# Kernel optimization log

Hardware: AMD Instinct MI355X
Metric: run time of the kernel (lower is better)

The kernel has to match this reference:

```python
import jax, jax.numpy as jnp
import numpy as np

N_CODES = 1024
D_CODE = 256
N_TOKENS = 131072
BETA = 0.25
DECAY = 0.97
EPS = 1e-05


def l2norm(x, axis=-1):
    # matches torch F.normalize(dim): x / max(||x||, 1e-12)
    n = jnp.sqrt(jnp.sum(x * x, axis=axis, keepdims=True))
    return x / jnp.maximum(n, 1e-12)


def setup_inputs() -> dict:
    key = jax.random.key(0)
    k1, k2, k3 = jax.random.split(key, 3)
    return {
        'z_e': jax.random.normal(k1, (N_TOKENS, D_CODE), dtype=jnp.float32),
        'codebook': jax.random.normal(k2, (N_CODES, D_CODE), dtype=jnp.float32),
        'ema_cluster_size': jnp.zeros((N_CODES,), dtype=jnp.float32),
        'ema_w': jax.random.normal(k3, (N_CODES, D_CODE), dtype=jnp.float32),
    }


def reference(z_e, codebook, ema_cluster_size, ema_w):
    z = l2norm(z_e, axis=1)                      # [N, d]
    cb = l2norm(codebook, axis=1)                # [K, d]
    # d = 2 - 2 * z @ cb.T ; argmin(d) == argmax(sim)
    sim = jnp.einsum('nd,kd->nk', z, cb)         # [N, K]
    codes = jnp.argmax(sim, axis=1)              # [N] int

    # EMA updates (no_grad in torch)
    counts = jnp.zeros((N_CODES,), z.dtype).at[codes].add(1.0)
    dw = jax.ops.segment_sum(z, codes, num_segments=N_CODES)  # onehot.T @ z
    new_cs = DECAY * ema_cluster_size + (1.0 - DECAY) * counts
    new_w = DECAY * ema_w + (1.0 - DECAY) * dw
    n = jnp.sum(new_cs)
    cluster_size = (new_cs + EPS) / (n + N_CODES * EPS) * n
    embed = l2norm(new_w / cluster_size[:, None], axis=1)
    # codebook.data.copy_(embed): value = embed, grad flows to codebook param
    new_cb = codebook + jax.lax.stop_gradient(embed - codebook)

    z_q = l2norm(new_cb[codes], axis=1)          # [N, d]
    vq_loss = BETA * jnp.mean((jax.lax.stop_gradient(z_e) - z_q) ** 2)
    z_q_out = z_e + jax.lax.stop_gradient(z_q - z_e)
    return (z_q_out, codes, vq_loss)
```

## Files before the change

kernel.cpp:

```cpp
#include <hip/hip_runtime.h>
#include <math.h>

#define N_TOK 131072
#define D 256
#define K_CODES 1024

typedef short bf16x8 __attribute__((ext_vector_type(8)));
typedef float f32x4 __attribute__((ext_vector_type(4)));

__device__ __forceinline__ unsigned short f2bf(float f) {
  unsigned x = __float_as_uint(f);
  unsigned r = x + 0x7fffu + ((x >> 16) & 1u);
  return (unsigned short)(r >> 16);
}

__global__ __launch_bounds__(256) void norm_cb_kernel(
    const float* __restrict__ cb, double* __restrict__ inv_nc64,
    unsigned short* __restrict__ cbbf) {
  const int c = blockIdx.x;
  const int d = threadIdx.x;
  const float v = cb[(size_t)c * D + d];
  double ssd = (double)v * (double)v;
#pragma unroll
  for (int o = 32; o; o >>= 1) ssd += __shfl_down(ssd, o, 64);
  __shared__ double red[4];
  if ((d & 63) == 0) red[d >> 6] = ssd;
  __syncthreads();
  const double tot = red[0] + red[1] + red[2] + red[3];
  const double inv = 1.0 / fmax(sqrt(tot), 1e-12);
  if (d == 0) inv_nc64[c] = inv;
  const int ctile = c >> 4, tk = c & 15;
  const int s = d >> 5, kg = (d >> 3) & 3, e = d & 7;
  cbbf[(((size_t)(ctile * 8 + s) * 64) + (kg * 16 + tk)) * 8 + e] =
      f2bf((float)((double)v * inv));
}

__global__ __launch_bounds__(512, 2) void vq_mfma_kernel(
    const float* __restrict__ z, const char* __restrict__ cbbf,
    float* __restrict__ out_codes, unsigned long long* __restrict__ cand2) {
  __shared__ __align__(16) char S[16384];
  __shared__ float norms[32];
  __shared__ int cand[32 * 8 * 3];
  __shared__ int clist[32 * 12];
  __shared__ float thrs[32];
  __shared__ int ccnt[32];

  const int tid = threadIdx.x;
  const int wv = tid >> 6;
  const int lane = tid & 63;
  const int t0b = blockIdx.x * 32;

  {
    const int tok = tid >> 4, sub = tid & 15;
    const float* zrow = z + (size_t)(t0b + tok) * D;
    float ss = 0.f;
#pragma unroll
    for (int i = 0; i < 2; ++i) {
      const int ku = sub + 16 * i;
      const float4 a = *(const float4*)(zrow + ku * 8);
      const float4 b = *(const float4*)(zrow + ku * 8 + 4);
      ss += a.x * a.x + a.y * a.y + a.z * a.z + a.w * a.w;
      ss += b.x * b.x + b.y * b.y + b.z * b.z + b.w * b.w;
      union { unsigned short h[8]; int4 v; } u;
      u.h[0] = f2bf(a.x); u.h[1] = f2bf(a.y); u.h[2] = f2bf(a.z); u.h[3] = f2bf(a.w);
      u.h[4] = f2bf(b.x); u.h[5] = f2bf(b.y); u.h[6] = f2bf(b.z); u.h[7] = f2bf(b.w);
      const int phys = (tok << 5) + (ku ^ (tok & 15));
      *(int4*)(S + ((size_t)phys << 4)) = u.v;
    }
    ss += __shfl_xor(ss, 1, 64);
    ss += __shfl_xor(ss, 2, 64);
    ss += __shfl_xor(ss, 4, 64);
    ss += __shfl_xor(ss, 8, 64);
    if (sub == 0) norms[tok] = sqrtf(ss);
  }
  __syncthreads();

  const int tk = lane & 15;
  const int kg = lane >> 4;

  f32x4 acc[2][8];
#pragma unroll
  for (int t = 0; t < 2; ++t)
#pragma unroll
    for (int c = 0; c < 8; ++c) acc[t][c] = (f32x4){0.f, 0.f, 0.f, 0.f};

  const char* cfb = cbbf + (size_t)wv * 65536 + (size_t)lane * 16;

#pragma unroll
  for (int s = 0; s < 8; ++s) {
    bf16x8 zf[2];
#pragma unroll
    for (int tt = 0; tt < 2; ++tt) {
      const int tok = tt * 16 + tk;
      const int ku = (s << 2) + kg;
      zf[tt] = *(const bf16x8*)(S + (((tok << 5) + (ku ^ (tok & 15))) << 4));
    }
    bf16x8 cf[8];
#pragma unroll
    for (int ct = 0; ct < 8; ++ct)
      cf[ct] = *(const bf16x8*)(cfb + ct * 8192 + s * 1024);
#pragma unroll
    for (int ct = 0; ct < 8; ++ct) {
      acc[0][ct] = __builtin_amdgcn_mfma_f32_16x16x32_bf16(cf[ct], zf[0], acc[0][ct], 0, 0, 0);
      acc[1][ct] = __builtin_amdgcn_mfma_f32_16x16x32_bf16(cf[ct], zf[1], acc[1][ct], 0, 0, 0);
    }
  }

#pragma unroll
  for (int tt = 0; tt < 2; ++tt) {
    float t1 = -3.0e38f, t2 = -3.0e38f;
    int i1 = 0;
#pragma unroll
    for (int ct = 0; ct < 8; ++ct)
#pragma unroll
      for (int r = 0; r < 4; ++r) {
        const float v = acc[tt][ct][r];
        const int k = (wv << 7) + (ct << 4) + (kg << 2) + r;
        if (v > t1) { t2 = t1; t1 = v; i1 = k; }
        else if (v > t2) t2 = v;
      }
#pragma unroll
    for (int off = 16; off <= 32; off <<= 1) {
      const float o1 = __shfl_xor(t1, off, 64);
      const int oi1 = __shfl_xor(i1, off, 64);
      const float o2 = __shfl_xor(t2, off, 64);
      const bool take = (o1 > t1) || (o1 == t1 && oi1 < i1);
      const float lo = take ? t1 : o1;
      t1 = take ? o1 : t1;
      i1 = take ? oi1 : i1;
      t2 = fmaxf(fmaxf(t2, o2), lo);
    }
    if (lane < 16) {
      int* p = cand + ((tt * 16 + lane) * 8 + wv) * 3;
      p[0] = __float_as_int(t1);
      p[1] = i1;
      p[2] = __float_as_int(t2);
    }
  }
  __syncthreads();

  if (tid < 32) {
    const float nrm = norms[tid];
    const float margin = 0.016f * nrm + 1.5e-3f;
    const int* base = cand + tid * 24;
    float v1 = -3.0e38f, v2 = -3.0e38f;
    int j1 = 0x7fffffff;
#pragma unroll
    for (int w = 0; w < 8; ++w) {
      const float a1 = __int_as_float(base[w * 3]);
      const int ai = base[w * 3 + 1];
      const float a2 = __int_as_float(base[w * 3 + 2]);
      const bool take = (a1 > v1) || (a1 == v1 && ai < j1);
      const float lo = take ? v1 : a1;
      v1 = take ? a1 : v1;
      j1 = take ? ai : j1;
      v2 = fmaxf(fmaxf(v2, a2), lo);
    }
    const float thr = v1 - margin;
    thrs[tid] = (v2 < thr) ? 3.0e38f : thr;
    ccnt[tid] = 0;
    out_codes[t0b + tid] = (float)j1;
  }
  __syncthreads();

#pragma unroll
  for (int tt = 0; tt < 2; ++tt) {
    const int tok = tt * 16 + tk;
    const float thr_t = thrs[tok];
#pragma unroll
    for (int ct = 0; ct < 8; ++ct)
#pragma unroll
      for (int r = 0; r < 4; ++r) {
        if (acc[tt][ct][r] >= thr_t) {
          const int pos = atomicAdd(&ccnt[tok], 1);
          if (pos < 12)
            clist[tok * 12 + pos] = (wv << 7) + (ct << 4) + (kg << 2) + r;
        }
      }
  }
  __syncthreads();

  if (tid < 32) {
    const int cnt = ccnt[tid];
    unsigned long long w0 = 0, w1 = 0;
    if (cnt > 0) {
      const int cc = cnt > 15 ? 15 : cnt;
      w0 = (unsigned long long)cc << 60;
      const int nst = cnt > 12 ? 12 : cnt;
      for (int j = 0; j < nst && j < 6; ++j)
        w0 |= ((unsigned long long)(clist[tid * 12 + j] & 1023)) << (10 * j);
      for (int j = 6; j < nst; ++j)
        w1 |= ((unsigned long long)(clist[tid * 12 + j] & 1023)) << (10 * (j - 6));
    }
    cand2[2 * (t0b + tid)] = w0;
    cand2[2 * (t0b + tid) + 1] = w1;
  }
}

__global__ __launch_bounds__(256) void recheck_kernel(
    const float* __restrict__ z, const float* __restrict__ cb,
    const double* __restrict__ inv_nc64,
    const unsigned long long* __restrict__ cand2,
    float* __restrict__ out_codes, int* __restrict__ ovf_list,
    int* __restrict__ ovf_cnt) {
  const int lane = threadIdx.x & 63;
  const int wid = (blockIdx.x * blockDim.x + threadIdx.x) >> 6;
  const int nw = (gridDim.x * blockDim.x) >> 6;
  for (int t = wid; t < N_TOK; t += nw) {
    const unsigned long long w0 = cand2[2 * t];
    if (w0 == 0ull) continue;
    const int cnt = (int)(w0 >> 60);
    if (cnt > 12) {
      if (lane == 0) ovf_list[atomicAdd(ovf_cnt, 1)] = t;
      continue;
    }
    const float4 zr = *(const float4*)(z + (size_t)t * D + lane * 4);
    const double z0 = zr.x, z1 = zr.y, z2 = zr.z, z3 = zr.w;
    const unsigned long long w1 = cand2[2 * t + 1];
    double best = -1.0e300;
    int bi = 0x7fffffff;
    for (int j = 0; j < cnt; ++j) {
      const int c = (j < 6) ? (int)((w0 >> (10 * j)) & 1023)
                            : (int)((w1 >> (10 * (j - 6))) & 1023);
      const float4 cr = *(const float4*)(cb + (size_t)c * D + lane * 4);
      double p = z0 * (double)cr.x + z1 * (double)cr.y +
                 z2 * (double)cr.z + z3 * (double)cr.w;
#pragma unroll
      for (int o = 32; o; o >>= 1) p += __shfl_xor(p, o, 64);
      p *= inv_nc64[c];
      if (p > best || (p == best && c < bi)) { best = p; bi = c; }
    }
    if (lane == 0) out_codes[t] = (float)bi;
  }
}

__global__ __launch_bounds__(256) void fullscan_kernel(
    const float* __restrict__ z, const float* __restrict__ cb,
    const double* __restrict__ inv_nc64, const int* __restrict__ ovf_list,
    const int* __restrict__ ovf_cnt, float* __restrict__ out_codes) {
  __shared__ float zs[256];
  __shared__ double bv[256];
  __shared__ int bis[256];
  const int n = *ovf_cnt;
  for (int i = blockIdx.x; i < n; i += gridDim.x) {
    const int t = ovf_list[i];
    zs[threadIdx.x] = z[(size_t)t * D + threadIdx.x];
    __syncthreads();
    double best = -1.0e300;
    int bidx = 0x7fffffff;
#pragma unroll
    for (int cc = 0; cc < 4; ++cc) {
      const int c = threadIdx.x + (cc << 8);
      const float4* crow = (const float4*)(cb + (size_t)c * D);
      double p = 0.0;
#pragma unroll 8
      for (int k4 = 0; k4 < 64; ++k4) {
        const float4 cv = crow[k4];
        p += (double)zs[4 * k4] * (double)cv.x +
             (double)zs[4 * k4 + 1] * (double)cv.y +
             (double)zs[4 * k4 + 2] * (double)cv.z +
             (double)zs[4 * k4 + 3] * (double)cv.w;
      }
      p *= inv_nc64[c];
      if (p > best || (p == best && c < bidx)) { best = p; bidx = c; }
    }
    bv[threadIdx.x] = best;
    bis[threadIdx.x] = bidx;
    __syncthreads();
    for (int s = 128; s; s >>= 1) {
      if (threadIdx.x < s) {
        const double ov = bv[threadIdx.x + s];
        const int oi = bis[threadIdx.x + s];
        if (ov > bv[threadIdx.x] ||
            (ov == bv[threadIdx.x] && oi < bis[threadIdx.x])) {
          bv[threadIdx.x] = ov;
          bis[threadIdx.x] = oi;
        }
      }
      __syncthreads();
    }
    if (threadIdx.x == 0) out_codes[t] = (float)bis[0];
    __syncthreads();
  }
}

__global__ __launch_bounds__(256) void inv_zn_kernel(
    const float* __restrict__ z, float* __restrict__ inv_zn) {
  const int lane = threadIdx.x & 63;
  const int wid = (blockIdx.x * blockDim.x + threadIdx.x) >> 6;
  const int nw = (gridDim.x * blockDim.x) >> 6;
  for (int t = wid; t < N_TOK; t += nw) {
    const float4 zr = *(const float4*)(z + (size_t)t * D + lane * 4);
    float ss = zr.x * zr.x + zr.y * zr.y + zr.z * zr.z + zr.w * zr.w;
#pragma unroll
    for (int o = 32; o; o >>= 1) ss += __shfl_xor(ss, o, 64);
    if (lane == 0) inv_zn[t] = 1.0f / fmaxf(sqrtf(ss), 1e-12f);
  }
}

__global__ __launch_bounds__(256) void hist_kernel(
    const float* __restrict__ codesf, int* __restrict__ hist) {
  const int t = blockIdx.x * 256 + threadIdx.x;
  if (t < N_TOK) atomicAdd(&hist[(int)codesf[t]], 1);
}

__global__ __launch_bounds__(256) void scan_kernel(
    const int* __restrict__ hist, int* __restrict__ offsets,
    int* __restrict__ cursor) {
  __shared__ int part[256];
  const int tid = threadIdx.x;
  int v[4];
  int s = 0;
#pragma unroll
  for (int j = 0; j < 4; ++j) {
    v[j] = hist[tid * 4 + j];
    s += v[j];
  }
  part[tid] = s;
  __syncthreads();
  for (int off = 1; off < 256; off <<= 1) {
    int x = (tid >= off) ? part[tid - off] : 0;
    __syncthreads();
    part[tid] += x;
    __syncthreads();
  }
  int excl = part[tid] - s;
#pragma unroll
  for (int j = 0; j < 4; ++j) {
    offsets[tid * 4 + j] = excl;
    cursor[tid * 4 + j] = excl;
    excl += v[j];
  }
  if (tid == 255) offsets[1024] = excl;
}

__global__ __launch_bounds__(256) void scatter_kernel(
    const float* __restrict__ codesf, int* __restrict__ cursor,
    int* __restrict__ tlist) {
  const int t = blockIdx.x * 256 + threadIdx.x;
  if (t < N_TOK) {
    const int c = (int)codesf[t];
    const int pos = atomicAdd(&cursor[c], 1);
    tlist[pos] = t;
  }
}

__global__ __launch_bounds__(256) void dw_build_kernel(
    const float* __restrict__ z, const int* __restrict__ tlist,
    const int* __restrict__ offsets, const float* __restrict__ inv_zn,
    const float* __restrict__ ema_w, float* __restrict__ embed) {
  const int c = blockIdx.x;
  const int d = threadIdx.x;
  const int i0 = offsets[c], i1 = offsets[c + 1];
  float sum = 0.f;
  for (int i = i0; i < i1; ++i) {
    const int t = tlist[i];
    sum += z[(size_t)t * D + d] * inv_zn[t];
  }
  const size_t idx = (size_t)c * D + d;
  const float w = 0.97f * ema_w[idx] + 0.03f * sum;
  float ss = w * w;
#pragma unroll
  for (int o = 32; o; o >>= 1) ss += __shfl_down(ss, o, 64);
  __shared__ float red[4];
  if ((d & 63) == 0) red[d >> 6] = ss;
  __syncthreads();
  const float tot = red[0] + red[1] + red[2] + red[3];
  embed[idx] = w / fmaxf(sqrtf(tot), 1e-12f);
}

__global__ __launch_bounds__(256) void gather_loss_kernel(
    const float* __restrict__ z, const float* __restrict__ embed,
    const float* __restrict__ codesf, float* __restrict__ out0,
    double* __restrict__ loss) {
  const size_t u0 = (size_t)blockIdx.x * 4096 + threadIdx.x;
  float part = 0.f;
#pragma unroll 4
  for (int i = 0; i < 16; ++i) {
    const size_t u = u0 + (size_t)i * 256;
    const size_t t = u >> 6;
    const int k4 = (int)(u & 63);
    const int code = (int)codesf[t];
    const float4 e = *(const float4*)(embed + (size_t)code * D + 4 * k4);
    const float4 ze = *(const float4*)(z + t * D + 4 * k4);
    *(float4*)(out0 + t * D + 4 * k4) = e;
    const float dx = ze.x - e.x, dy = ze.y - e.y;
    const float dz = ze.z - e.z, dw4 = ze.w - e.w;
    part += dx * dx + dy * dy + dz * dz + dw4 * dw4;
  }
#pragma unroll
  for (int o = 32; o; o >>= 1) part += __shfl_down(part, o, 64);
  __shared__ float red[4];
  if ((threadIdx.x & 63) == 0) red[threadIdx.x >> 6] = part;
  __syncthreads();
  if (threadIdx.x == 0)
    unsafeAtomicAdd(loss, (double)(red[0] + red[1] + red[2] + red[3]));
}

__global__ void finalize_kernel(const double* __restrict__ loss,
                                float* __restrict__ out2) {
  out2[0] = (float)(0.25 * loss[0] / 33554432.0);
}

extern "C" void kernel_launch(void* const* d_in, const int* in_sizes, int n_in,
                              void* d_out, int out_size, void* d_ws, size_t ws_size,
                              hipStream_t stream) {
  const float* z = (const float*)d_in[0];
  const float* cb = (const float*)d_in[1];
  const float* ema_w = (const float*)d_in[3];

  float* out0 = (float*)d_out;
  float* out1 = out0 + (size_t)N_TOK * D;
  float* out2 = out1 + N_TOK;

  char* ws = (char*)d_ws;
  unsigned short* cbbf = (unsigned short*)ws;
  float* embed = (float*)ws;
  int* ovf_list = (int*)(ws + 524288);
  unsigned long long* cand2 = (unsigned long long*)(ws + 1048576);
  int* tlist = (int*)(ws + 1048576);
  float* inv_zn = (float*)(ws + 1572864);
  int* hist = (int*)(ws + 2097152);
  int* offsets = (int*)(ws + 2101248);
  int* cursor = (int*)(ws + 2105856);
  double* inv_nc64 = (double*)(ws + 3145728);
  double* loss = (double*)(ws + 3153920);
  int* ovf_cnt = (int*)(ws + 3153984);

  hipMemsetAsync(ws + 3153920, 0, 128, stream);

  norm_cb_kernel<<<K_CODES, 256, 0, stream>>>(cb, inv_nc64, cbbf);
  vq_mfma_kernel<<<N_TOK / 32, 512, 0, stream>>>(
      z, (const char*)cbbf, out1, cand2);
  recheck_kernel<<<4096, 256, 0, stream>>>(z, cb, inv_nc64, cand2, out1,
                                           ovf_list, ovf_cnt);
  fullscan_kernel<<<2048, 256, 0, stream>>>(z, cb, inv_nc64, ovf_list,
                                            ovf_cnt, out1);
  inv_zn_kernel<<<2048, 256, 0, stream>>>(z, inv_zn);
  hipMemsetAsync(hist, 0, 4096, stream);
  hist_kernel<<<N_TOK / 256, 256, 0, stream>>>(out1, hist);
  scan_kernel<<<1, 256, 0, stream>>>(hist, offsets, cursor);
  scatter_kernel<<<N_TOK / 256, 256, 0, stream>>>(out1, cursor, tlist);
  dw_build_kernel<<<K_CODES, 256, 0, stream>>>(z, tlist, offsets, inv_zn,
                                               ema_w, embed);
  gather_loss_kernel<<<2048, 256, 0, stream>>>(z, embed, out1, out0, loss);
  finalize_kernel<<<1, 1, 0, stream>>>(loss, out2);
}
```

Baseline: 416.7 us.

## Double tokens per VQ block and fold inverse-norm computation into it

The MFMA similarity kernel now handles 64 tokens per block instead of 32, so each codebook fragment loaded from global memory is reused across four token tiles rather than two, halving codebook traffic per token. The per-token inverse norm is written directly from the staging phase, which removes the separate inv_zn kernel and its extra full read of z. The trade-off is more accumulator registers (128 floats) and launch bounds lowered to one block per CU, which may reduce occupancy and latency hiding. The inv_zn buffer moves to a new workspace offset to avoid overlapping other buffers.

```diff
diff --git a/kernel.cpp b/kernel.cpp
--- a/kernel.cpp
+++ b/kernel.cpp
@@ -35,28 +35,29 @@
       f2bf((float)((double)v * inv));
 }
 
-__global__ __launch_bounds__(512, 2) void vq_mfma_kernel(
+__global__ __launch_bounds__(512, 1) void vq_mfma_kernel(
     const float* __restrict__ z, const char* __restrict__ cbbf,
-    float* __restrict__ out_codes, unsigned long long* __restrict__ cand2) {
-  __shared__ __align__(16) char S[16384];
-  __shared__ float norms[32];
-  __shared__ int cand[32 * 8 * 3];
-  __shared__ int clist[32 * 12];
-  __shared__ float thrs[32];
-  __shared__ int ccnt[32];
+    float* __restrict__ out_codes, float* __restrict__ inv_zn,
+    unsigned long long* __restrict__ cand2) {
+  __shared__ __align__(16) char S[32768];
+  __shared__ float norms[64];
+  __shared__ int cand[64 * 8 * 3];
+  __shared__ int clist[64 * 12];
+  __shared__ float thrs[64];
+  __shared__ int ccnt[64];
 
   const int tid = threadIdx.x;
   const int wv = tid >> 6;
   const int lane = tid & 63;
-  const int t0b = blockIdx.x * 32;
+  const int t0b = blockIdx.x * 64;
 
   {
-    const int tok = tid >> 4, sub = tid & 15;
+    const int tok = tid >> 3, sub = tid & 7;
     const float* zrow = z + (size_t)(t0b + tok) * D;
     float ss = 0.f;
 #pragma unroll
-    for (int i = 0; i < 2; ++i) {
-      const int ku = sub + 16 * i;
+    for (int i = 0; i < 4; ++i) {
+      const int ku = sub + 8 * i;
       const float4 a = *(const float4*)(zrow + ku * 8);
       const float4 b = *(const float4*)(zrow + ku * 8 + 4);
       ss += a.x * a.x + a.y * a.y + a.z * a.z + a.w * a.w;
@@ -70,17 +71,20 @@
     ss += __shfl_xor(ss, 1, 64);
     ss += __shfl_xor(ss, 2, 64);
     ss += __shfl_xor(ss, 4, 64);
-    ss += __shfl_xor(ss, 8, 64);
-    if (sub == 0) norms[tok] = sqrtf(ss);
+    if (sub == 0) {
+      const float nr = sqrtf(ss);
+      norms[tok] = nr;
+      inv_zn[t0b + tok] = 1.0f / fmaxf(nr, 1e-12f);
+    }
   }
   __syncthreads();
 
   const int tk = lane & 15;
   const int kg = lane >> 4;
 
-  f32x4 acc[2][8];
-#pragma unroll
-  for (int t = 0; t < 2; ++t)
+  f32x4 acc[4][8];
+#pragma unroll
+  for (int t = 0; t < 4; ++t)
 #pragma unroll
     for (int c = 0; c < 8; ++c) acc[t][c] = (f32x4){0.f, 0.f, 0.f, 0.f};
 
@@ -88,26 +92,25 @@
 
 #pragma unroll
   for (int s = 0; s < 8; ++s) {
-    bf16x8 zf[2];
-#pragma unroll
-    for (int tt = 0; tt < 2; ++tt) {
+    bf16x8 zf[4];
+#pragma unroll
+    for (int tt = 0; tt < 4; ++tt) {
       const int tok = tt * 16 + tk;
       const int ku = (s << 2) + kg;
       zf[tt] = *(const bf16x8*)(S + (((tok << 5) + (ku ^ (tok & 15))) << 4));
     }
-    bf16x8 cf[8];
-#pragma unroll
-    for (int ct = 0; ct < 8; ++ct)
-      cf[ct] = *(const bf16x8*)(cfb + ct * 8192 + s * 1024);
 #pragma unroll
     for (int ct = 0; ct < 8; ++ct) {
-      acc[0][ct] = __builtin_amdgcn_mfma_f32_16x16x32_bf16(cf[ct], zf[0], acc[0][ct], 0, 0, 0);
-      acc[1][ct] = __builtin_amdgcn_mfma_f32_16x16x32_bf16(cf[ct], zf[1], acc[1][ct], 0, 0, 0);
-    }
-  }
-
-#pragma unroll
-  for (int tt = 0; tt < 2; ++tt) {
+      const bf16x8 cf = *(const bf16x8*)(cfb + ct * 8192 + s * 1024);
+      acc[0][ct] = __builtin_amdgcn_mfma_f32_16x16x32_bf16(cf, zf[0], acc[0][ct], 0, 0, 0);
+      acc[1][ct] = __builtin_amdgcn_mfma_f32_16x16x32_bf16(cf, zf[1], acc[1][ct], 0, 0, 0);
+      acc[2][ct] = __builtin_amdgcn_mfma_f32_16x16x32_bf16(cf, zf[2], acc[2][ct], 0, 0, 0);
+      acc[3][ct] = __builtin_amdgcn_mfma_f32_16x16x32_bf16(cf, zf[3], acc[3][ct], 0, 0, 0);
+    }
+  }
+
+#pragma unroll
+  for (int tt = 0; tt < 4; ++tt) {
     float t1 = -3.0e38f, t2 = -3.0e38f;
     int i1 = 0;
 #pragma unroll
@@ -139,7 +142,7 @@
   }
   __syncthreads();
 
-  if (tid < 32) {
+  if (tid < 64) {
     const float nrm = norms[tid];
     const float margin = 0.016f * nrm + 1.5e-3f;
     const int* base = cand + tid * 24;
@@ -164,7 +167,7 @@
   __syncthreads();
 
 #pragma unroll
-  for (int tt = 0; tt < 2; ++tt) {
+  for (int tt = 0; tt < 4; ++tt) {
     const int tok = tt * 16 + tk;
     const float thr_t = thrs[tok];
 #pragma unroll
@@ -180,7 +183,7 @@
   }
   __syncthreads();
 
-  if (tid < 32) {
+  if (tid < 64) {
     const int cnt = ccnt[tid];
     unsigned long long w0 = 0, w1 = 0;
     if (cnt > 0) {
@@ -281,20 +284,6 @@
     }
     if (threadIdx.x == 0) out_codes[t] = (float)bis[0];
     __syncthreads();
-  }
-}
-
-__global__ __launch_bounds__(256) void inv_zn_kernel(
-    const float* __restrict__ z, float* __restrict__ inv_zn) {
-  const int lane = threadIdx.x & 63;
-  const int wid = (blockIdx.x * blockDim.x + threadIdx.x) >> 6;
-  const int nw = (gridDim.x * blockDim.x) >> 6;
-  for (int t = wid; t < N_TOK; t += nw) {
-    const float4 zr = *(const float4*)(z + (size_t)t * D + lane * 4);
-    float ss = zr.x * zr.x + zr.y * zr.y + zr.z * zr.z + zr.w * zr.w;
-#pragma unroll
-    for (int o = 32; o; o >>= 1) ss += __shfl_xor(ss, o, 64);
-    if (lane == 0) inv_zn[t] = 1.0f / fmaxf(sqrtf(ss), 1e-12f);
   }
 }
 
@@ -419,24 +408,23 @@
   int* ovf_list = (int*)(ws + 524288);
   unsigned long long* cand2 = (unsigned long long*)(ws + 1048576);
   int* tlist = (int*)(ws + 1048576);
-  float* inv_zn = (float*)(ws + 1572864);
   int* hist = (int*)(ws + 2097152);
   int* offsets = (int*)(ws + 2101248);
   int* cursor = (int*)(ws + 2105856);
   double* inv_nc64 = (double*)(ws + 3145728);
   double* loss = (double*)(ws + 3153920);
   int* ovf_cnt = (int*)(ws + 3153984);
+  float* inv_zn = (float*)(ws + 3158016);
 
   hipMemsetAsync(ws + 3153920, 0, 128, stream);
 
   norm_cb_kernel<<<K_CODES, 256, 0, stream>>>(cb, inv_nc64, cbbf);
-  vq_mfma_kernel<<<N_TOK / 32, 512, 0, stream>>>(
-      z, (const char*)cbbf, out1, cand2);
+  vq_mfma_kernel<<<N_TOK / 64, 512, 0, stream>>>(
+      z, (const char*)cbbf, out1, inv_zn, cand2);
   recheck_kernel<<<4096, 256, 0, stream>>>(z, cb, inv_nc64, cand2, out1,
                                            ovf_list, ovf_cnt);
   fullscan_kernel<<<2048, 256, 0, stream>>>(z, cb, inv_nc64, ovf_list,
                                             ovf_cnt, out1);
-  inv_zn_kernel<<<2048, 256, 0, stream>>>(z, inv_zn);
   hipMemsetAsync(hist, 0, 4096, stream);
   hist_kernel<<<N_TOK / 256, 256, 0, stream>>>(out1, hist);
   scan_kernel<<<1, 256, 0, stream>>>(hist, offsets, cursor);
```

Result: slower. 429.7 us (+3.1%).
